# Optimization experiments

Measured on AMD Instinct MI355X. Metric: run time of the kernel, lower is better.

The kernel has to match this reference:

```python
import jax, jax.numpy as jnp
import numpy as np

N_NODES = 100000   # users + items
EMB_DIM = 64
N_EDGES = 3200000  # avg degree 32
N_LAYERS = 3


def setup_inputs() -> dict:
    key = jax.random.key(0)
    k1, k2, k3, k4 = jax.random.split(key, 4)
    emb = jax.random.normal(k1, (N_NODES, EMB_DIM), dtype=jnp.float32)
    rows = jax.random.randint(k2, (N_EDGES,), 0, N_NODES, dtype=jnp.int32)
    cols = jax.random.randint(k3, (N_EDGES,), 0, N_NODES, dtype=jnp.int32)
    vals = jax.random.uniform(k4, (N_EDGES,), dtype=jnp.float32)
    return {"ItemAndUserEmebddings": emb, "adj_rows": rows,
            "adj_cols": cols, "adj_vals": vals}


def _spmm(rows, cols, vals, x):
    # (sparse A) @ x : gather source rows, scale by edge value, scatter-add to dest
    msgs = vals[:, None] * x[cols]                      # [E, d]
    return jax.ops.segment_sum(msgs, rows, num_segments=x.shape[0])


def reference(ItemAndUserEmebddings, adj_rows, adj_cols, adj_vals):
    all_emb = ItemAndUserEmebddings
    embeddings_list = [all_emb]
    for _ in range(N_LAYERS):
        all_emb = _spmm(adj_rows, adj_cols, adj_vals, all_emb)
        embeddings_list.append(all_emb)
    stacked = jnp.stack(embeddings_list, axis=1)        # [N, L+1, d]
    lightgcn_all_embeddings = jnp.mean(stacked, axis=1)  # [N, d]
    return (lightgcn_all_embeddings, stacked)
```

## Files before the change

kernel.cpp:

```cpp
#include <hip/hip_runtime.h>
#include <hip/hip_fp16.h>

#define N_NODES 100000
#define EMB_DIM 64
#define N_EDGES 3200000
#define N_LAYERS 3

#define SCAN_BLOCK 512
#define N_SCAN_BLOCKS ((N_NODES + SCAN_BLOCK - 1) / SCAN_BLOCK)

#define ABINROWS 256
#define NBINS ((N_NODES + ABINROWS - 1) / ABINROWS)
#define NBINS_P 512
#define ACHUNK 2048
#define AEPT 8
#define NCHUNKS ((N_EDGES + ACHUNK - 1) / ACHUNK)
#define BCHUNK 4096
#define NBCHUNKS ((N_EDGES + BCHUNK - 1) / BCHUNK)


typedef float f32x4 __attribute__((ext_vector_type(4)));
typedef unsigned short u16x4 __attribute__((ext_vector_type(4)));

__device__ __forceinline__ unsigned short f32_to_bf16_rtn(float f) {
    unsigned u = __float_as_uint(f);
    unsigned r = u + 0x7FFFu + ((u >> 16) & 1u);
    return (unsigned short)(r >> 16);
}
__device__ __forceinline__ float bf16_to_f32(unsigned short h) {
    return __uint_as_float(((unsigned)h) << 16);
}


__global__ void __launch_bounds__(256) bin_count(const int* __restrict__ rows,
                                                 int* __restrict__ binCounts) {
    __shared__ int h[NBINS];
    int t = threadIdx.x;
    for (int i = t; i < NBINS; i += 256) h[i] = 0;
    __syncthreads();
    int base = blockIdx.x * BCHUNK;
    int n = N_EDGES - base; if (n > BCHUNK) n = BCHUNK;
    for (int i = t; i < n; i += 256)
        atomicAdd(&h[__builtin_nontemporal_load(rows + base + i) >> 8], 1);
    __syncthreads();
    for (int i = t; i < NBINS; i += 256) {
        int c = h[i];
        if (c) atomicAdd(&binCounts[i], c);
    }
}

__global__ void __launch_bounds__(512) bin_scan(const int* __restrict__ binCounts,
                                                int* __restrict__ binPtr) {
    __shared__ int sm[512];
    int t = threadIdx.x;
    int v = (t < NBINS) ? binCounts[t] : 0;
    sm[t] = v;
    __syncthreads();
    for (int off = 1; off < 512; off <<= 1) {
        int u = (t >= off) ? sm[t - off] : 0;
        __syncthreads();
        sm[t] += u;
        __syncthreads();
    }
    if (t < NBINS) binPtr[t + 1] = sm[t];
    if (t == 0) binPtr[0] = 0;
}


__global__ void count_rows(const int* __restrict__ rows, int* __restrict__ counts) {
    int e = blockIdx.x * blockDim.x + threadIdx.x;
    if (e >= N_EDGES) return;
    atomicAdd(&counts[rows[e]], 1);
}

__global__ void __launch_bounds__(SCAN_BLOCK) scan_phase1(const int* __restrict__ counts,
                                                          int* __restrict__ blockSums) {
    __shared__ int sm[SCAN_BLOCK];
    int idx = blockIdx.x * SCAN_BLOCK + threadIdx.x;
    int v = (idx < N_NODES) ? counts[idx] : 0;
    sm[threadIdx.x] = v;
    __syncthreads();
    for (int off = SCAN_BLOCK / 2; off > 0; off >>= 1) {
        if (threadIdx.x < off) sm[threadIdx.x] += sm[threadIdx.x + off];
        __syncthreads();
    }
    if (threadIdx.x == 0) blockSums[blockIdx.x] = sm[0];
}

__global__ void __launch_bounds__(256) scan_phase2(const int* __restrict__ blockSums,
                                                   int* __restrict__ blockOffs,
                                                   int* __restrict__ row_ptr) {
    __shared__ int sm[256];
    int t = threadIdx.x;
    int v = (t < N_SCAN_BLOCKS) ? blockSums[t] : 0;
    sm[t] = v;
    __syncthreads();
    for (int off = 1; off < 256; off <<= 1) {
        int u = (t >= off) ? sm[t - off] : 0;
        __syncthreads();
        sm[t] += u;
        __syncthreads();
    }
    if (t < N_SCAN_BLOCKS) blockOffs[t] = (t == 0) ? 0 : sm[t - 1];
    if (t == 255) row_ptr[N_NODES] = sm[255];
}

__global__ void __launch_bounds__(SCAN_BLOCK) scan_phase3(const int* __restrict__ counts,
                                                          const int* __restrict__ blockOffs,
                                                          int* __restrict__ row_ptr) {
    __shared__ int sm[SCAN_BLOCK];
    int idx = blockIdx.x * SCAN_BLOCK + threadIdx.x;
    int t = threadIdx.x;
    int v = (idx < N_NODES) ? counts[idx] : 0;
    sm[t] = v;
    __syncthreads();
    for (int off = 1; off < SCAN_BLOCK; off <<= 1) {
        int u = (t >= off) ? sm[t - off] : 0;
        __syncthreads();
        sm[t] += u;
        __syncthreads();
    }
    if (idx < N_NODES) row_ptr[idx] = blockOffs[blockIdx.x] + sm[t] - v;
}


__global__ void __launch_bounds__(256) build_sortA(const int* __restrict__ rows,
                                                   const int* __restrict__ cols,
                                                   const float* __restrict__ vals,
                                                   const int* __restrict__ binPtr,
                                                   int* __restrict__ bucketFill,
                                                   uint2* __restrict__ records) {
    __shared__ int binCnt[NBINS_P];
    __shared__ int binInc[NBINS_P];
    __shared__ int binCur[NBINS_P];
    __shared__ int binG[NBINS];
    __shared__ uint2 buf[ACHUNK];

    int base = blockIdx.x * ACHUNK;
    int n = N_EDGES - base; if (n > ACHUNK) n = ACHUNK;
    int t = threadIdx.x;

    for (int i = t; i < NBINS_P; i += 256) { binCnt[i] = 0; binCur[i] = 0; }
    __syncthreads();

    int r_[AEPT]; unsigned pk_[AEPT];
#pragma unroll AEPT
    for (int k = 0; k < AEPT; ++k) {
        int i = t + k * 256;
        r_[k] = 0; pk_[k] = 0;
        if (i < n) {
            int e = base + i;
            int r = __builtin_nontemporal_load(rows + e);
            unsigned hb = __half_as_ushort(__float2half(__builtin_nontemporal_load(vals + e)));
            r_[k] = r;
            pk_[k] = (((unsigned)__builtin_nontemporal_load(cols + e)) << 15) | (hb & 0x7FFFu);
            atomicAdd(&binCnt[r >> 8], 1);
        }
    }
    __syncthreads();

    binInc[t] = binCnt[t];
    binInc[t + 256] = binCnt[t + 256];
    __syncthreads();
    for (int off = 1; off < NBINS_P; off <<= 1) {
        int i0 = t, i1 = t + 256;
        int v0 = (i0 >= off) ? binInc[i0 - off] : 0;
        int v1 = (i1 >= off) ? binInc[i1 - off] : 0;
        __syncthreads();
        binInc[i0] += v0;
        binInc[i1] += v1;
        __syncthreads();
    }

#pragma unroll AEPT
    for (int k = 0; k < AEPT; ++k) {
        int i = t + k * 256;
        if (i < n) {
            int b = r_[k] >> 8;
            int slot = (binInc[b] - binCnt[b]) + atomicAdd(&binCur[b], 1);
            buf[slot] = make_uint2((unsigned)r_[k], pk_[k]);
        }
    }
    for (int b = t; b < NBINS; b += 256) {
        int c = binCnt[b];
        if (c > 0) binG[b] = binPtr[b] + atomicAdd(&bucketFill[b], c);
    }
    __syncthreads();

    for (int p = t; p < n; p += 256) {
        uint2 rec = buf[p];
        int b = (int)(rec.x >> 8);
        int dst = binG[b] + (p - (binInc[b] - binCnt[b]));
        records[dst] = rec;
    }
}

__global__ void __launch_bounds__(256) build_phaseB(const int* __restrict__ binPtr,
                                                    const uint2* __restrict__ records,
                                                    unsigned* __restrict__ s_edges,
                                                    int* __restrict__ row_ptr) {
    __shared__ int lcnt[ABINROWS];
    __shared__ int linc[ABINROWS];
    __shared__ int lrp[ABINROWS];
    __shared__ int lfill[ABINROWS];
    int b = blockIdx.x;
    int t = threadIdx.x;
    int r0 = b * ABINROWS;
    int r1 = r0 + ABINROWS; if (r1 > N_NODES) r1 = N_NODES;
    int nr = r1 - r0;
    int beg = binPtr[b];
    int end = binPtr[b + 1];

    lcnt[t] = 0; lfill[t] = 0;
    __syncthreads();
    for (int i = beg + t; i < end; i += 256) {
        atomicAdd(&lcnt[(int)records[i].x - r0], 1);
    }
    __syncthreads();
    linc[t] = lcnt[t];
    __syncthreads();
    for (int off = 1; off < 256; off <<= 1) {
        int u = (t >= off) ? linc[t - off] : 0;
        __syncthreads();
        linc[t] += u;
        __syncthreads();
    }
    lrp[t] = beg + linc[t] - lcnt[t];
    if (t < nr) row_ptr[r0 + t] = lrp[t];
    if (t == 0) row_ptr[r0 + nr] = end;
    __syncthreads();
    for (int i = beg + t; i < end; i += 256) {
        uint2 rec = records[i];
        int lr = (int)rec.x - r0;
        int lp = atomicAdd(&lfill[lr], 1);
        s_edges[lrp[lr] + lp] = rec.y;
    }
}

__global__ void emb_to_bf16(const float* __restrict__ emb, unsigned short* __restrict__ mirror) {
    int t = blockIdx.x * blockDim.x + threadIdx.x;
    if (t >= N_NODES * 16) return;
    f32x4 v = __builtin_nontemporal_load((const f32x4*)emb + t);
    u16x4 o;
    o.x = f32_to_bf16_rtn(v.x); o.y = f32_to_bf16_rtn(v.y);
    o.z = f32_to_bf16_rtn(v.z); o.w = f32_to_bf16_rtn(v.w);
    __builtin_nontemporal_store(o, (u16x4*)mirror + t);
}


__device__ __forceinline__ void gacc(float4& acc, unsigned p, int j,
                                     const unsigned short* __restrict__ srcMirror) {
    float v = __half2float(__ushort_as_half((unsigned short)(p & 0x7FFFu)));
    ushort4 m = *(const ushort4*)(srcMirror + (size_t)(p >> 15) * 64 + j * 4);
    acc.x += v * bf16_to_f32(m.x);
    acc.y += v * bf16_to_f32(m.y);
    acc.z += v * bf16_to_f32(m.z);
    acc.w += v * bf16_to_f32(m.w);
}

__device__ __forceinline__ float4 spmm_row_core(int beg, int end, int g, int j, int lane,
                                                const unsigned* __restrict__ s_edges,
                                                const unsigned short* __restrict__ srcMirror) {
    int deg = end - beg;
    unsigned ew = (lane < deg) ? __builtin_nontemporal_load(s_edges + beg + lane) : 0u;
    float4 acc = make_float4(0.f, 0.f, 0.f, 0.f);
    int nfull = deg < 64 ? deg : 64;
    for (int kb = 0; kb < nfull; kb += 16) {
        int k0 = kb + g, k1 = kb + g + 4, k2 = kb + g + 8, k3 = kb + g + 12;
        unsigned p0 = __shfl(ew, k0);
        unsigned p1 = __shfl(ew, k1);
        unsigned p2 = __shfl(ew, k2);
        unsigned p3 = __shfl(ew, k3);
        if (k0 < nfull) gacc(acc, p0, j, srcMirror);
        if (k1 < nfull) gacc(acc, p1, j, srcMirror);
        if (k2 < nfull) gacc(acc, p2, j, srcMirror);
        if (k3 < nfull) gacc(acc, p3, j, srcMirror);
    }
    for (int e = beg + 64 + g; e < end; e += 4) {
        unsigned p = s_edges[e];
        gacc(acc, p, j, srcMirror);
    }
    acc.x += __shfl_xor(acc.x, 16); acc.y += __shfl_xor(acc.y, 16);
    acc.z += __shfl_xor(acc.z, 16); acc.w += __shfl_xor(acc.w, 16);
    acc.x += __shfl_xor(acc.x, 32); acc.y += __shfl_xor(acc.y, 32);
    acc.z += __shfl_xor(acc.z, 32); acc.w += __shfl_xor(acc.w, 32);
    return acc;
}

__global__ void __launch_bounds__(256) spmm_gather_bf16_mid(const int* __restrict__ row_ptr,
                                                            const unsigned* __restrict__ s_edges,
                                                            const unsigned short* __restrict__ srcMirror,
                                                            float* __restrict__ dstStacked,
                                                            unsigned short* __restrict__ dstMirror) {
    int wave = (blockIdx.x * blockDim.x + threadIdx.x) >> 6;
    if (wave >= N_NODES) return;
    int lane = threadIdx.x & 63;
    int g = lane >> 4, j = lane & 15;
    float4 acc = spmm_row_core(row_ptr[wave], row_ptr[wave + 1], g, j, lane, s_edges, srcMirror);
    if (lane < 16) {
        f32x4 vv = {acc.x, acc.y, acc.z, acc.w};
        __builtin_nontemporal_store(vv, (f32x4*)(dstStacked + (size_t)wave * 256 + j * 4));
        u16x4 o;
        o.x = f32_to_bf16_rtn(acc.x); o.y = f32_to_bf16_rtn(acc.y);
        o.z = f32_to_bf16_rtn(acc.z); o.w = f32_to_bf16_rtn(acc.w);
        __builtin_nontemporal_store(o, (u16x4*)(dstMirror + (size_t)wave * 64 + j * 4));
    }
}

__global__ void __launch_bounds__(256) spmm_gather_bf16_last(const int* __restrict__ row_ptr,
                                                             const unsigned* __restrict__ s_edges,
                                                             const unsigned short* __restrict__ srcMirror,
                                                             const float* __restrict__ emb,
                                                             float* __restrict__ stacked,
                                                             float* __restrict__ meanOut) {
    int wave = (blockIdx.x * blockDim.x + threadIdx.x) >> 6;
    if (wave >= N_NODES) return;
    int lane = threadIdx.x & 63;
    int g = lane >> 4, j = lane & 15;
    float4 acc = spmm_row_core(row_ptr[wave], row_ptr[wave + 1], g, j, lane, s_edges, srcMirror);
    if (lane < 16) {
        float* base = stacked + (size_t)wave * 256 + j * 4;
        f32x4 a  = __builtin_nontemporal_load((const f32x4*)(emb + (size_t)wave * 64 + j * 4));
        f32x4 b1 = __builtin_nontemporal_load((const f32x4*)(base + 64));
        f32x4 c2 = __builtin_nontemporal_load((const f32x4*)(base + 128));
        f32x4 d3 = {acc.x, acc.y, acc.z, acc.w};
        __builtin_nontemporal_store(a, (f32x4*)base);
        __builtin_nontemporal_store(d3, (f32x4*)(base + 192));
        f32x4 s;
        s.x = 0.25f * (a.x + b1.x + c2.x + d3.x);
        s.y = 0.25f * (a.y + b1.y + c2.y + d3.y);
        s.z = 0.25f * (a.z + b1.z + c2.z + d3.z);
        s.w = 0.25f * (a.w + b1.w + c2.w + d3.w);
        __builtin_nontemporal_store(s, (f32x4*)(meanOut + (size_t)wave * 64 + j * 4));
    }
}

__global__ void mean_layers(const float* __restrict__ emb,
                            float* __restrict__ stacked,
                            float* __restrict__ meanOut) {
    int t = blockIdx.x * blockDim.x + threadIdx.x;
    if (t >= N_NODES * 16) return;
    int n = t >> 4;
    int j = t & 15;
    float4* base = (float4*)stacked + (size_t)n * 64;
    float4 a = ((const float4*)emb)[t];
    float4 b = base[16 + j];
    float4 c = base[32 + j];
    float4 d = base[48 + j];
    base[j] = a;
    float4 s;
    s.x = 0.25f * (a.x + b.x + c.x + d.x);
    s.y = 0.25f * (a.y + b.y + c.y + d.y);
    s.z = 0.25f * (a.z + b.z + c.z + d.z);
    s.w = 0.25f * (a.w + b.w + c.w + d.w);
    ((float4*)meanOut)[t] = s;
}


__global__ void scatter_edges_int2(const int* __restrict__ rows, const int* __restrict__ cols,
                                   const float* __restrict__ vals,
                                   const int* __restrict__ row_ptr, int* __restrict__ fill,
                                   int2* __restrict__ s_colval) {
    int e = blockIdx.x * blockDim.x + threadIdx.x;
    if (e >= N_EDGES) return;
    int r = rows[e];
    int pos = row_ptr[r] + atomicAdd(&fill[r], 1);
    int2 p; p.x = cols[e]; p.y = __float_as_int(vals[e]);
    s_colval[pos] = p;
}

__global__ void __launch_bounds__(256) spmm_gather_f32(const int* __restrict__ row_ptr,
                                                       const int2* __restrict__ s_colval,
                                                       const float* __restrict__ src, int srcStride,
                                                       float* __restrict__ dst) {
    int wave = (blockIdx.x * blockDim.x + threadIdx.x) >> 6;
    if (wave >= N_NODES) return;
    int lane = threadIdx.x & 63;
    int g = lane >> 4, j = lane & 15;
    int beg = row_ptr[wave], end = row_ptr[wave + 1];
    float4 acc = make_float4(0.f, 0.f, 0.f, 0.f);
    int e = beg + g;
    for (; e + 4 < end; e += 8) {
        int2 p0 = s_colval[e], p1 = s_colval[e + 4];
        float v0 = __int_as_float(p0.y), v1 = __int_as_float(p1.y);
        float4 m0 = *(const float4*)(src + (size_t)p0.x * srcStride + j * 4);
        float4 m1 = *(const float4*)(src + (size_t)p1.x * srcStride + j * 4);
        acc.x += v0 * m0.x + v1 * m1.x; acc.y += v0 * m0.y + v1 * m1.y;
        acc.z += v0 * m0.z + v1 * m1.z; acc.w += v0 * m0.w + v1 * m1.w;
    }
    for (; e < end; e += 4) {
        int2 p = s_colval[e];
        float v = __int_as_float(p.y);
        float4 m = *(const float4*)(src + (size_t)p.x * srcStride + j * 4);
        acc.x += v * m.x; acc.y += v * m.y; acc.z += v * m.z; acc.w += v * m.w;
    }
    acc.x += __shfl_xor(acc.x, 16); acc.y += __shfl_xor(acc.y, 16);
    acc.z += __shfl_xor(acc.z, 16); acc.w += __shfl_xor(acc.w, 16);
    acc.x += __shfl_xor(acc.x, 32); acc.y += __shfl_xor(acc.y, 32);
    acc.z += __shfl_xor(acc.z, 32); acc.w += __shfl_xor(acc.w, 32);
    if (lane < 16)
        *(float4*)(dst + (size_t)wave * 256 + j * 4) = acc;
}


__global__ void init_stacked_full(const float* __restrict__ emb, float* __restrict__ stacked) {
    int t = blockIdx.x * blockDim.x + threadIdx.x;
    if (t >= N_NODES * 64) return;
    int n = t >> 6, j = t & 63;
    float4 v = (j < 16) ? ((const float4*)emb)[n * 16 + j] : make_float4(0.f, 0.f, 0.f, 0.f);
    ((float4*)stacked)[n * 64 + j] = v;
}

__global__ void spmm_atomic(const int* __restrict__ rows, const int* __restrict__ cols,
                            const float* __restrict__ vals, float* __restrict__ stacked,
                            int lprev) {
    int t = blockIdx.x * blockDim.x + threadIdx.x;
    int e = t >> 4, j = t & 15;
    if (e >= N_EDGES) return;
    int r = rows[e], c = cols[e];
    float v = vals[e];
    const float4* src = (const float4*)(stacked + (size_t)c * 256 + lprev * 64);
    float4 m = src[j];
    float* dst = stacked + (size_t)r * 256 + (lprev + 1) * 64 + j * 4;
    atomicAdd(dst + 0, v * m.x); atomicAdd(dst + 1, v * m.y);
    atomicAdd(dst + 2, v * m.z); atomicAdd(dst + 3, v * m.w);
}

__global__ void mean_layers_plain(const float* __restrict__ stacked, float* __restrict__ meanOut) {
    int t = blockIdx.x * blockDim.x + threadIdx.x;
    if (t >= N_NODES * 16) return;
    int n = t >> 4, j = t & 15;
    const float4* base = (const float4*)(stacked + (size_t)n * 256);
    float4 a = base[j], b = base[16 + j], c = base[32 + j], d = base[48 + j];
    float4 s;
    s.x = 0.25f * (a.x + b.x + c.x + d.x);
    s.y = 0.25f * (a.y + b.y + c.y + d.y);
    s.z = 0.25f * (a.z + b.z + c.z + d.z);
    s.w = 0.25f * (a.w + b.w + c.w + d.w);
    ((float4*)meanOut)[t] = s;
}

extern "C" void kernel_launch(void* const* d_in, const int* in_sizes, int n_in,
                              void* d_out, int out_size, void* d_ws, size_t ws_size,
                              hipStream_t stream) {
    const float* emb  = (const float*)d_in[0];
    const int*   rows = (const int*)d_in[1];
    const int*   cols = (const int*)d_in[2];
    const float* vals = (const float*)d_in[3];

    float* meanOut = (float*)d_out;
    float* stacked = (float*)d_out + (size_t)N_NODES * EMB_DIM;

    const size_t headInts = (size_t)(N_NODES * 2 + 1 + 2 * N_SCAN_BLOCKS);
    size_t need_bf16 = headInts * sizeof(int) + 64
                     + (size_t)N_EDGES * sizeof(unsigned)
                     + 2 * (size_t)N_NODES * EMB_DIM * sizeof(unsigned short);
    size_t need_f32  = headInts * sizeof(int) + 64 + (size_t)N_EDGES * sizeof(int2);

    if (ws_size >= need_bf16) {
        char* w = (char*)d_ws;
        int* counts    = (int*)w;  w += (size_t)N_NODES * sizeof(int);
        int* row_ptr   = (int*)w;  w += (size_t)(N_NODES + 1) * sizeof(int);
        int* blockSums = (int*)w;  w += (size_t)N_SCAN_BLOCKS * sizeof(int);
        int* blockOffs = (int*)w;  w += (size_t)N_SCAN_BLOCKS * sizeof(int);
        w = (char*)(((uintptr_t)w + 15) & ~(uintptr_t)15);
        unsigned* s_edges = (unsigned*)w;  w += (size_t)N_EDGES * sizeof(unsigned);
        unsigned short* mirrorA = (unsigned short*)w;  w += (size_t)N_NODES * EMB_DIM * sizeof(unsigned short);
        unsigned short* mirrorB = (unsigned short*)w;
        uint2* records = (uint2*)mirrorA;
        int* binCounts  = counts;
        int* bucketFill = counts + NBINS;
        int* binPtr     = counts + 2 * NBINS;

        hipMemsetAsync(counts, 0, (size_t)(2 * NBINS) * sizeof(int), stream);
        bin_count<<<NBCHUNKS, 256, 0, stream>>>(rows, binCounts);
        bin_scan<<<1, 512, 0, stream>>>(binCounts, binPtr);
        build_sortA<<<NCHUNKS, 256, 0, stream>>>(rows, cols, vals, binPtr, bucketFill, records);
        build_phaseB<<<NBINS, 256, 0, stream>>>(binPtr, records, s_edges, row_ptr);
        {
            int total = N_NODES * 16;
            int block = 256, grid = (total + block - 1) / block;
            emb_to_bf16<<<grid, block, 0, stream>>>(emb, mirrorA);
        }
        {
            long long threads = (long long)N_NODES * 64;
            int block = 256;
            int grid = (int)((threads + block - 1) / block);
            spmm_gather_bf16_mid<<<grid, block, 0, stream>>>(row_ptr, s_edges, mirrorA, stacked + 1 * 64, mirrorB);
            spmm_gather_bf16_mid<<<grid, block, 0, stream>>>(row_ptr, s_edges, mirrorB, stacked + 2 * 64, mirrorA);
            spmm_gather_bf16_last<<<grid, block, 0, stream>>>(row_ptr, s_edges, mirrorA, emb, stacked, meanOut);
        }
    } else if (ws_size >= need_f32) {
        char* w = (char*)d_ws;
        int* counts    = (int*)w;  w += (size_t)N_NODES * sizeof(int);
        int* row_ptr   = (int*)w;  w += (size_t)(N_NODES + 1) * sizeof(int);
        int* blockSums = (int*)w;  w += (size_t)N_SCAN_BLOCKS * sizeof(int);
        int* blockOffs = (int*)w;  w += (size_t)N_SCAN_BLOCKS * sizeof(int);
        w = (char*)(((uintptr_t)w + 15) & ~(uintptr_t)15);
        int2* s_colval = (int2*)w;

        hipMemsetAsync(counts, 0, (size_t)N_NODES * sizeof(int), stream);
        {
            int block = 256, grid = (N_EDGES + block - 1) / block;
            count_rows<<<grid, block, 0, stream>>>(rows, counts);
        }
        scan_phase1<<<N_SCAN_BLOCKS, SCAN_BLOCK, 0, stream>>>(counts, blockSums);
        scan_phase2<<<1, 256, 0, stream>>>(blockSums, blockOffs, row_ptr);
        scan_phase3<<<N_SCAN_BLOCKS, SCAN_BLOCK, 0, stream>>>(counts, blockOffs, row_ptr);
        hipMemsetAsync(counts, 0, (size_t)N_NODES * sizeof(int), stream);
        {
            int block = 256, grid = (N_EDGES + block - 1) / block;
            scatter_edges_int2<<<grid, block, 0, stream>>>(rows, cols, vals, row_ptr, counts, s_colval);
        }
        {
            long long threads = (long long)N_NODES * 64;
            int block = 256;
            int grid = (int)((threads + block - 1) / block);
            spmm_gather_f32<<<grid, block, 0, stream>>>(row_ptr, s_colval, emb, 64, stacked + 1 * 64);
            spmm_gather_f32<<<grid, block, 0, stream>>>(row_ptr, s_colval, stacked + 1 * 64, 256, stacked + 2 * 64);
            spmm_gather_f32<<<grid, block, 0, stream>>>(row_ptr, s_colval, stacked + 2 * 64, 256, stacked + 3 * 64);
        }
        {
            int total = N_NODES * 16;
            int block = 256, grid = (total + block - 1) / block;
            mean_layers<<<grid, block, 0, stream>>>(emb, stacked, meanOut);
        }
    } else {
        {
            int total = N_NODES * 64;
            int block = 256, grid = (total + block - 1) / block;
            init_stacked_full<<<grid, block, 0, stream>>>(emb, stacked);
        }
        {
            long long total = (long long)N_EDGES * 16;
            int block = 256, grid = (int)((total + block - 1) / block);
            for (int l = 0; l < N_LAYERS; ++l)
                spmm_atomic<<<grid, block, 0, stream>>>(rows, cols, vals, stacked, l);
        }
        {
            int total = N_NODES * 16;
            int block = 256, grid = (total + block - 1) / block;
            mean_layers_plain<<<grid, block, 0, stream>>>(stacked, meanOut);
        }
    }
}
```

Before: 572.9 us.

## Partition SpMM by source-node range into four passes for cache locality

The CSR build now splits each row's edges into four segments by source-node range, producing a row pointer with four entries per row. Each SpMM layer becomes four passes, each gathering only from a quarter of the bf16 source mirror. The aim is to keep the gather working set small enough to stay in cache, cutting random-gather misses. In exchange each layer re-reads and rewrites the fp32 accumulator three extra times, reads a row pointer four times as large, and adds many kernel launches. It also gives poorer wave utilisation, since each row segment holds only about 8 edges.

```diff
diff --git a/kernel.cpp b/kernel.cpp
--- a/kernel.cpp
+++ b/kernel.cpp
@@ -17,6 +17,9 @@
 #define NCHUNKS ((N_EDGES + ACHUNK - 1) / ACHUNK)
 #define BCHUNK 4096
 #define NBCHUNKS ((N_EDGES + BCHUNK - 1) / BCHUNK)
+
+#define NPART 4
+#define PART_DIV 25000
 
 
 typedef float f32x4 __attribute__((ext_vector_type(4)));
@@ -198,11 +201,11 @@
 __global__ void __launch_bounds__(256) build_phaseB(const int* __restrict__ binPtr,
                                                     const uint2* __restrict__ records,
                                                     unsigned* __restrict__ s_edges,
-                                                    int* __restrict__ row_ptr) {
-    __shared__ int lcnt[ABINROWS];
-    __shared__ int linc[ABINROWS];
-    __shared__ int lrp[ABINROWS];
-    __shared__ int lfill[ABINROWS];
+                                                    int* __restrict__ rp2) {
+    __shared__ int lcnt[ABINROWS * NPART];
+    __shared__ int lseg[ABINROWS * NPART];
+    __shared__ int lfill[ABINROWS * NPART];
+    __shared__ int tot[256];
     int b = blockIdx.x;
     int t = threadIdx.x;
     int r0 = b * ABINROWS;
@@ -211,29 +214,37 @@
     int beg = binPtr[b];
     int end = binPtr[b + 1];
 
-    lcnt[t] = 0; lfill[t] = 0;
-    __syncthreads();
-    for (int i = beg + t; i < end; i += 256) {
-        atomicAdd(&lcnt[(int)records[i].x - r0], 1);
-    }
-    __syncthreads();
-    linc[t] = lcnt[t];
-    __syncthreads();
-    for (int off = 1; off < 256; off <<= 1) {
-        int u = (t >= off) ? linc[t - off] : 0;
-        __syncthreads();
-        linc[t] += u;
-        __syncthreads();
-    }
-    lrp[t] = beg + linc[t] - lcnt[t];
-    if (t < nr) row_ptr[r0 + t] = lrp[t];
-    if (t == 0) row_ptr[r0 + nr] = end;
+    for (int i = t; i < ABINROWS * NPART; i += 256) { lcnt[i] = 0; lfill[i] = 0; }
     __syncthreads();
     for (int i = beg + t; i < end; i += 256) {
         uint2 rec = records[i];
-        int lr = (int)rec.x - r0;
-        int lp = atomicAdd(&lfill[lr], 1);
-        s_edges[lrp[lr] + lp] = rec.y;
+        int p = (int)(rec.y >> 15) / PART_DIV;
+        atomicAdd(&lcnt[((int)rec.x - r0) * NPART + p], 1);
+    }
+    __syncthreads();
+    int c0 = lcnt[4 * t + 0], c1 = lcnt[4 * t + 1], c2 = lcnt[4 * t + 2], c3 = lcnt[4 * t + 3];
+    int lsum = c0 + c1 + c2 + c3;
+    tot[t] = lsum;
+    __syncthreads();
+    for (int off = 1; off < 256; off <<= 1) {
+        int u = (t >= off) ? tot[t - off] : 0;
+        __syncthreads();
+        tot[t] += u;
+        __syncthreads();
+    }
+    int excl = tot[t] - lsum;
+    lseg[4 * t + 0] = beg + excl;
+    lseg[4 * t + 1] = beg + excl + c0;
+    lseg[4 * t + 2] = beg + excl + c0 + c1;
+    lseg[4 * t + 3] = beg + excl + c0 + c1 + c2;
+    __syncthreads();
+    for (int i = t; i < nr * NPART; i += 256) rp2[r0 * NPART + i] = lseg[i];
+    if (b == NBINS - 1 && t == 0) rp2[N_NODES * NPART] = end;
+    for (int i = beg + t; i < end; i += 256) {
+        uint2 rec = records[i];
+        int idx = ((int)rec.x - r0) * NPART + (int)(rec.y >> 15) / PART_DIV;
+        int lp = atomicAdd(&lfill[idx], 1);
+        s_edges[lseg[idx] + lp] = rec.y;
     }
 }
 
@@ -287,43 +298,56 @@
     return acc;
 }
 
-__global__ void __launch_bounds__(256) spmm_gather_bf16_mid(const int* __restrict__ row_ptr,
-                                                            const unsigned* __restrict__ s_edges,
-                                                            const unsigned short* __restrict__ srcMirror,
-                                                            float* __restrict__ dstStacked,
-                                                            unsigned short* __restrict__ dstMirror) {
+__global__ void __launch_bounds__(256) spmm_pass(const int* __restrict__ rp2,
+                                                 const unsigned* __restrict__ s_edges,
+                                                 const unsigned short* __restrict__ srcMirror,
+                                                 int p, int accum,
+                                                 float* __restrict__ dst,
+                                                 unsigned short* __restrict__ dstMirror) {
     int wave = (blockIdx.x * blockDim.x + threadIdx.x) >> 6;
     if (wave >= N_NODES) return;
     int lane = threadIdx.x & 63;
     int g = lane >> 4, j = lane & 15;
-    float4 acc = spmm_row_core(row_ptr[wave], row_ptr[wave + 1], g, j, lane, s_edges, srcMirror);
+    int beg = rp2[wave * NPART + p];
+    int end = rp2[wave * NPART + p + 1];
+    float4 acc = spmm_row_core(beg, end, g, j, lane, s_edges, srcMirror);
     if (lane < 16) {
+        float* out = dst + (size_t)wave * 256 + j * 4;
+        if (accum) {
+            f32x4 prev = __builtin_nontemporal_load((const f32x4*)out);
+            acc.x += prev.x; acc.y += prev.y; acc.z += prev.z; acc.w += prev.w;
+        }
         f32x4 vv = {acc.x, acc.y, acc.z, acc.w};
-        __builtin_nontemporal_store(vv, (f32x4*)(dstStacked + (size_t)wave * 256 + j * 4));
-        u16x4 o;
-        o.x = f32_to_bf16_rtn(acc.x); o.y = f32_to_bf16_rtn(acc.y);
-        o.z = f32_to_bf16_rtn(acc.z); o.w = f32_to_bf16_rtn(acc.w);
-        __builtin_nontemporal_store(o, (u16x4*)(dstMirror + (size_t)wave * 64 + j * 4));
-    }
-}
-
-__global__ void __launch_bounds__(256) spmm_gather_bf16_last(const int* __restrict__ row_ptr,
-                                                             const unsigned* __restrict__ s_edges,
-                                                             const unsigned short* __restrict__ srcMirror,
-                                                             const float* __restrict__ emb,
-                                                             float* __restrict__ stacked,
-                                                             float* __restrict__ meanOut) {
+        __builtin_nontemporal_store(vv, (f32x4*)out);
+        if (dstMirror) {
+            u16x4 o;
+            o.x = f32_to_bf16_rtn(acc.x); o.y = f32_to_bf16_rtn(acc.y);
+            o.z = f32_to_bf16_rtn(acc.z); o.w = f32_to_bf16_rtn(acc.w);
+            __builtin_nontemporal_store(o, (u16x4*)(dstMirror + (size_t)wave * 64 + j * 4));
+        }
+    }
+}
+
+__global__ void __launch_bounds__(256) spmm_last_final(const int* __restrict__ rp2,
+                                                       const unsigned* __restrict__ s_edges,
+                                                       const unsigned short* __restrict__ srcMirror,
+                                                       const float* __restrict__ emb,
+                                                       float* __restrict__ stacked,
+                                                       float* __restrict__ meanOut) {
     int wave = (blockIdx.x * blockDim.x + threadIdx.x) >> 6;
     if (wave >= N_NODES) return;
     int lane = threadIdx.x & 63;
     int g = lane >> 4, j = lane & 15;
-    float4 acc = spmm_row_core(row_ptr[wave], row_ptr[wave + 1], g, j, lane, s_edges, srcMirror);
+    int beg = rp2[wave * NPART + 3];
+    int end = rp2[wave * NPART + 4];
+    float4 acc = spmm_row_core(beg, end, g, j, lane, s_edges, srcMirror);
     if (lane < 16) {
         float* base = stacked + (size_t)wave * 256 + j * 4;
+        f32x4 prev = __builtin_nontemporal_load((const f32x4*)(base + 192));
+        f32x4 d3 = {acc.x + prev.x, acc.y + prev.y, acc.z + prev.z, acc.w + prev.w};
         f32x4 a  = __builtin_nontemporal_load((const f32x4*)(emb + (size_t)wave * 64 + j * 4));
         f32x4 b1 = __builtin_nontemporal_load((const f32x4*)(base + 64));
         f32x4 c2 = __builtin_nontemporal_load((const f32x4*)(base + 128));
-        f32x4 d3 = {acc.x, acc.y, acc.z, acc.w};
         __builtin_nontemporal_store(a, (f32x4*)base);
         __builtin_nontemporal_store(d3, (f32x4*)(base + 192));
         f32x4 s;
@@ -451,32 +475,31 @@
     float* meanOut = (float*)d_out;
     float* stacked = (float*)d_out + (size_t)N_NODES * EMB_DIM;
 
-    const size_t headInts = (size_t)(N_NODES * 2 + 1 + 2 * N_SCAN_BLOCKS);
-    size_t need_bf16 = headInts * sizeof(int) + 64
+    const size_t headInts2 = (size_t)(N_NODES * NPART + 1 + 3 * NBINS + 1);
+    size_t need_bf16 = headInts2 * sizeof(int) + 64
                      + (size_t)N_EDGES * sizeof(unsigned)
                      + 2 * (size_t)N_NODES * EMB_DIM * sizeof(unsigned short);
+    const size_t headInts = (size_t)(N_NODES * 2 + 1 + 2 * N_SCAN_BLOCKS);
     size_t need_f32  = headInts * sizeof(int) + 64 + (size_t)N_EDGES * sizeof(int2);
 
     if (ws_size >= need_bf16) {
         char* w = (char*)d_ws;
-        int* counts    = (int*)w;  w += (size_t)N_NODES * sizeof(int);
-        int* row_ptr   = (int*)w;  w += (size_t)(N_NODES + 1) * sizeof(int);
-        int* blockSums = (int*)w;  w += (size_t)N_SCAN_BLOCKS * sizeof(int);
-        int* blockOffs = (int*)w;  w += (size_t)N_SCAN_BLOCKS * sizeof(int);
+        int* rp2 = (int*)w;  w += (size_t)(N_NODES * NPART + 1) * sizeof(int);
+        int* binCounts  = (int*)w;
+        int* bucketFill = binCounts + NBINS;
+        int* binPtr     = binCounts + 2 * NBINS;
+        w += (size_t)(3 * NBINS + 1) * sizeof(int);
         w = (char*)(((uintptr_t)w + 15) & ~(uintptr_t)15);
         unsigned* s_edges = (unsigned*)w;  w += (size_t)N_EDGES * sizeof(unsigned);
         unsigned short* mirrorA = (unsigned short*)w;  w += (size_t)N_NODES * EMB_DIM * sizeof(unsigned short);
         unsigned short* mirrorB = (unsigned short*)w;
         uint2* records = (uint2*)mirrorA;
-        int* binCounts  = counts;
-        int* bucketFill = counts + NBINS;
-        int* binPtr     = counts + 2 * NBINS;
-
-        hipMemsetAsync(counts, 0, (size_t)(2 * NBINS) * sizeof(int), stream);
+
+        hipMemsetAsync(binCounts, 0, (size_t)(2 * NBINS) * sizeof(int), stream);
         bin_count<<<NBCHUNKS, 256, 0, stream>>>(rows, binCounts);
         bin_scan<<<1, 512, 0, stream>>>(binCounts, binPtr);
         build_sortA<<<NCHUNKS, 256, 0, stream>>>(rows, cols, vals, binPtr, bucketFill, records);
-        build_phaseB<<<NBINS, 256, 0, stream>>>(binPtr, records, s_edges, row_ptr);
+        build_phaseB<<<NBINS, 256, 0, stream>>>(binPtr, records, s_edges, rp2);
         {
             int total = N_NODES * 16;
             int block = 256, grid = (total + block - 1) / block;
@@ -486,9 +509,18 @@
             long long threads = (long long)N_NODES * 64;
             int block = 256;
             int grid = (int)((threads + block - 1) / block);
-            spmm_gather_bf16_mid<<<grid, block, 0, stream>>>(row_ptr, s_edges, mirrorA, stacked + 1 * 64, mirrorB);
-            spmm_gather_bf16_mid<<<grid, block, 0, stream>>>(row_ptr, s_edges, mirrorB, stacked + 2 * 64, mirrorA);
-            spmm_gather_bf16_last<<<grid, block, 0, stream>>>(row_ptr, s_edges, mirrorA, emb, stacked, meanOut);
+            spmm_pass<<<grid, block, 0, stream>>>(rp2, s_edges, mirrorA, 0, 0, stacked + 64, nullptr);
+            spmm_pass<<<grid, block, 0, stream>>>(rp2, s_edges, mirrorA, 1, 1, stacked + 64, nullptr);
+            spmm_pass<<<grid, block, 0, stream>>>(rp2, s_edges, mirrorA, 2, 1, stacked + 64, nullptr);
+            spmm_pass<<<grid, block, 0, stream>>>(rp2, s_edges, mirrorA, 3, 1, stacked + 64, mirrorB);
+            spmm_pass<<<grid, block, 0, stream>>>(rp2, s_edges, mirrorB, 0, 0, stacked + 128, nullptr);
+            spmm_pass<<<grid, block, 0, stream>>>(rp2, s_edges, mirrorB, 1, 1, stacked + 128, nullptr);
+            spmm_pass<<<grid, block, 0, stream>>>(rp2, s_edges, mirrorB, 2, 1, stacked + 128, nullptr);
+            spmm_pass<<<grid, block, 0, stream>>>(rp2, s_edges, mirrorB, 3, 1, stacked + 128, mirrorA);
+            spmm_pass<<<grid, block, 0, stream>>>(rp2, s_edges, mirrorA, 0, 0, stacked + 192, nullptr);
+            spmm_pass<<<grid, block, 0, stream>>>(rp2, s_edges, mirrorA, 1, 1, stacked + 192, nullptr);
+            spmm_pass<<<grid, block, 0, stream>>>(rp2, s_edges, mirrorA, 2, 1, stacked + 192, nullptr);
+            spmm_last_final<<<grid, block, 0, stream>>>(rp2, s_edges, mirrorA, emb, stacked, meanOut);
         }
     } else if (ws_size >= need_f32) {
         char* w = (char*)d_ws;
```

Measured after the change: 819.5 us. 43.1% more time.

## Replace shared-memory staged bin sort with direct atomic scatter to records

Applied to the files above, without the earlier changes.

The partial-bin sort kernel no longer stages records in an LDS buffer after a local prefix scan. Each block of 4096 edges now counts per-bin, reserves global ranges, then rereads rows, cols and vals and writes each record straight to its global slot via an LDS atomic cursor. This drops the block-level scan and LDS buffer and uses larger chunks, at the cost of reading rows twice and scattering writes with less coalescing.

```diff
diff --git a/kernel.cpp b/kernel.cpp
--- a/kernel.cpp
+++ b/kernel.cpp
@@ -11,10 +11,8 @@
 
 #define ABINROWS 256
 #define NBINS ((N_NODES + ABINROWS - 1) / ABINROWS)
-#define NBINS_P 512
-#define ACHUNK 2048
-#define AEPT 8
-#define NCHUNKS ((N_EDGES + ACHUNK - 1) / ACHUNK)
+#define ACH2 4096
+#define NCHUNKS2 ((N_EDGES + ACH2 - 1) / ACH2)
 #define BCHUNK 4096
 #define NBCHUNKS ((N_EDGES + BCHUNK - 1) / BCHUNK)
 
@@ -124,74 +122,36 @@
 }
 
 
-__global__ void __launch_bounds__(256) build_sortA(const int* __restrict__ rows,
+__global__ void __launch_bounds__(256) build_sort2(const int* __restrict__ rows,
                                                    const int* __restrict__ cols,
                                                    const float* __restrict__ vals,
                                                    const int* __restrict__ binPtr,
                                                    int* __restrict__ bucketFill,
                                                    uint2* __restrict__ records) {
-    __shared__ int binCnt[NBINS_P];
-    __shared__ int binInc[NBINS_P];
-    __shared__ int binCur[NBINS_P];
+    __shared__ int binCnt[NBINS];
+    __shared__ int binCur[NBINS];
     __shared__ int binG[NBINS];
-    __shared__ uint2 buf[ACHUNK];
-
-    int base = blockIdx.x * ACHUNK;
-    int n = N_EDGES - base; if (n > ACHUNK) n = ACHUNK;
+    int base = blockIdx.x * ACH2;
+    int n = N_EDGES - base; if (n > ACH2) n = ACH2;
     int t = threadIdx.x;
 
-    for (int i = t; i < NBINS_P; i += 256) { binCnt[i] = 0; binCur[i] = 0; }
-    __syncthreads();
-
-    int r_[AEPT]; unsigned pk_[AEPT];
-#pragma unroll AEPT
-    for (int k = 0; k < AEPT; ++k) {
-        int i = t + k * 256;
-        r_[k] = 0; pk_[k] = 0;
-        if (i < n) {
-            int e = base + i;
-            int r = __builtin_nontemporal_load(rows + e);
-            unsigned hb = __half_as_ushort(__float2half(__builtin_nontemporal_load(vals + e)));
-            r_[k] = r;
-            pk_[k] = (((unsigned)__builtin_nontemporal_load(cols + e)) << 15) | (hb & 0x7FFFu);
-            atomicAdd(&binCnt[r >> 8], 1);
-        }
-    }
-    __syncthreads();
-
-    binInc[t] = binCnt[t];
-    binInc[t + 256] = binCnt[t + 256];
-    __syncthreads();
-    for (int off = 1; off < NBINS_P; off <<= 1) {
-        int i0 = t, i1 = t + 256;
-        int v0 = (i0 >= off) ? binInc[i0 - off] : 0;
-        int v1 = (i1 >= off) ? binInc[i1 - off] : 0;
-        __syncthreads();
-        binInc[i0] += v0;
-        binInc[i1] += v1;
-        __syncthreads();
-    }
-
-#pragma unroll AEPT
-    for (int k = 0; k < AEPT; ++k) {
-        int i = t + k * 256;
-        if (i < n) {
-            int b = r_[k] >> 8;
-            int slot = (binInc[b] - binCnt[b]) + atomicAdd(&binCur[b], 1);
-            buf[slot] = make_uint2((unsigned)r_[k], pk_[k]);
-        }
-    }
+    for (int i = t; i < NBINS; i += 256) { binCnt[i] = 0; binCur[i] = 0; }
+    __syncthreads();
+    for (int i = t; i < n; i += 256) atomicAdd(&binCnt[rows[base + i] >> 8], 1);
+    __syncthreads();
     for (int b = t; b < NBINS; b += 256) {
         int c = binCnt[b];
-        if (c > 0) binG[b] = binPtr[b] + atomicAdd(&bucketFill[b], c);
-    }
-    __syncthreads();
-
-    for (int p = t; p < n; p += 256) {
-        uint2 rec = buf[p];
-        int b = (int)(rec.x >> 8);
-        int dst = binG[b] + (p - (binInc[b] - binCnt[b]));
-        records[dst] = rec;
+        if (c) binG[b] = binPtr[b] + atomicAdd(&bucketFill[b], c);
+    }
+    __syncthreads();
+    for (int i = t; i < n; i += 256) {
+        int e = base + i;
+        int r = rows[e];
+        int b = r >> 8;
+        unsigned hb = __half_as_ushort(__float2half(vals[e]));
+        unsigned pk = (((unsigned)cols[e]) << 15) | (hb & 0x7FFFu);
+        int pos = binG[b] + atomicAdd(&binCur[b], 1);
+        records[pos] = make_uint2((unsigned)r, pk);
     }
 }
 
@@ -475,7 +435,7 @@
         hipMemsetAsync(counts, 0, (size_t)(2 * NBINS) * sizeof(int), stream);
         bin_count<<<NBCHUNKS, 256, 0, stream>>>(rows, binCounts);
         bin_scan<<<1, 512, 0, stream>>>(binCounts, binPtr);
-        build_sortA<<<NCHUNKS, 256, 0, stream>>>(rows, cols, vals, binPtr, bucketFill, records);
+        build_sort2<<<NCHUNKS2, 256, 0, stream>>>(rows, cols, vals, binPtr, bucketFill, records);
         build_phaseB<<<NBINS, 256, 0, stream>>>(binPtr, records, s_edges, row_ptr);
         {
             int total = N_NODES * 16;
```

New measurement: 589.3 us. 1.03x slower.
